# Optimization experiments

Measured on AMD Instinct MI355X. Metric: run time of the kernel, lower is better.

Reference implementation:

```python
import jax, jax.numpy as jnp
import numpy as np
import math

DIM = 1024
N_HEADS = 16
HEAD_DIM = DIM // N_HEADS


def get_sin_cos(seq_len, dim):
    # theta: (dim/2,), freqs: (L, dim/2), emb: (L, dim)
    theta = 10000.0 ** (-jnp.arange(0, dim, 2, dtype=jnp.float32) / dim)
    position = jnp.arange(seq_len, dtype=jnp.float32)
    freqs = position[:, None] * theta[None, :]
    emb = jnp.concatenate([jnp.sin(freqs), jnp.cos(freqs)], axis=-1)
    sin = emb[None, None]  # (1,1,L,dim)
    cos = emb[None, None]
    return sin, cos


def rotate_half(x):
    x1, x2 = x[..., ::2], x[..., 1::2]
    return jnp.concatenate([-x2, x1], axis=-1)


def apply_rope(q, k):
    sin, cos = get_sin_cos(q.shape[2], q.shape[-1])
    q = q * cos + rotate_half(q) * sin
    k = k * cos + rotate_half(k) * sin
    return q, k


def setup_inputs() -> dict:
    key = jax.random.key(0)
    ks = jax.random.split(key, 3)
    B, L, D = 2, 2048, DIM
    x = jax.random.normal(ks[0], (B, L, D), dtype=jnp.float32)
    Wqkv = jax.random.normal(ks[1], (D, 3 * D), dtype=jnp.float32) * (1.0 / math.sqrt(D))
    bqkv = jnp.zeros((3 * D,), dtype=jnp.float32)
    Wout = jax.random.normal(ks[2], (D, D), dtype=jnp.float32) * (1.0 / math.sqrt(D))
    bout = jnp.zeros((D,), dtype=jnp.float32)
    return {"x": x, "Wqkv": Wqkv, "bqkv": bqkv, "Wout": Wout, "bout": bout}


def reference(x, Wqkv, bqkv, Wout, bout):
    B, L, D = x.shape
    H, Hd = N_HEADS, HEAD_DIM
    qkv = (x @ Wqkv + bqkv).reshape(B, L, 3, H, Hd)
    q, k, v = qkv[:, :, 0], qkv[:, :, 1], qkv[:, :, 2]  # (B,L,H,Hd)
    q = q.transpose(0, 2, 1, 3)  # (B,H,L,Hd)
    k = k.transpose(0, 2, 1, 3)
    v = v.transpose(0, 2, 1, 3)
    q, k = apply_rope(q, k)
    scores = jnp.einsum('bhqd,bhkd->bhqk', q, k) / math.sqrt(Hd)
    probs = jax.nn.softmax(scores, axis=-1)
    out = jnp.einsum('bhqk,bhkd->bhqd', probs, v)
    out = out.transpose(0, 2, 1, 3).reshape(B, L, D)
    return out @ Wout + bout
```

## Files before the change

kernel.cpp:

```cpp
#include <hip/hip_runtime.h>
#include <hip/hip_bf16.h>
#include <math.h>

typedef __bf16 bf16;
typedef __bf16 bf16x8 __attribute__((ext_vector_type(8)));
typedef __bf16 bf16x4 __attribute__((ext_vector_type(4)));
typedef float f32x4 __attribute__((ext_vector_type(4)));
typedef float f32x16 __attribute__((ext_vector_type(16)));

#define DEV __device__ __forceinline__
#define AS1(p) ((const __attribute__((address_space(1))) void*)(p))
#define AS3(p) ((__attribute__((address_space(3))) void*)(p))

#define Bsz 2
#define Lseq 2048
#define Dm 1024
#define Hh 16
#define HD 64
#define BL (Bsz * Lseq)
#define TN (3 * Dm)

#define LOG2E 1.44269504088896f

#define OFF_XATT  ((size_t)0)
#define OFF_WQKVT (OFF_XATT  + (size_t)BL * Dm * 2)
#define OFF_WOUTT (OFF_WQKVT + (size_t)TN * Dm * 2)
#define OFF_TAB   (OFF_WOUTT + (size_t)Dm * Dm * 2)
#define OFF_Q     (OFF_TAB   + (size_t)Lseq * 32 * 8)
#define OFF_K     (OFF_Q     + (size_t)BL * Dm * 2)
#define OFF_VT    (OFF_K     + (size_t)BL * Dm * 2)

DEV float exp2_fast(float x) {
    float r;
    asm("v_exp_f32 %0, %1" : "=v"(r) : "v"(x));
    return r;
}

__global__ __launch_bounds__(256) void k_convert(const float* __restrict__ in,
                                                 bf16* __restrict__ out) {
    int i = blockIdx.x * 256 + threadIdx.x;
    const float4* in4 = (const float4*)in;
    float4 a = in4[i * 2];
    float4 b = in4[i * 2 + 1];
    bf16x8 o;
    o[0] = (bf16)a.x; o[1] = (bf16)a.y; o[2] = (bf16)a.z; o[3] = (bf16)a.w;
    o[4] = (bf16)b.x; o[5] = (bf16)b.y; o[6] = (bf16)b.z; o[7] = (bf16)b.w;
    ((bf16x8*)out)[i] = o;
}

__global__ __launch_bounds__(256) void k_transpose(const float* __restrict__ in,
                                                   bf16* __restrict__ out,
                                                   int R, int C) {
    __shared__ float t[32][33];
    int bx = blockIdx.x * 32;
    int by = blockIdx.y * 32;
    int tx = threadIdx.x, ty = threadIdx.y;
#pragma unroll
    for (int i = 0; i < 32; i += 8)
        t[ty + i][tx] = in[(size_t)(by + ty + i) * C + bx + tx];
    __syncthreads();
#pragma unroll
    for (int i = 0; i < 32; i += 8)
        out[(size_t)(bx + ty + i) * R + by + tx] = (bf16)t[tx][ty + i];
}

__global__ __launch_bounds__(256) void k_sincos(float2* __restrict__ tab) {
    int idx = blockIdx.x * 256 + threadIdx.x;
    int pos = idx >> 5, t = idx & 31;
    float theta = powf(10000.0f, -(float)t * (1.0f / 32.0f));
    float f = (float)pos * theta;
    tab[idx] = make_float2(sinf(f), cosf(f));
}

template <int EPI>
DEV void gemm_body(const bf16* __restrict__ A,
                   const bf16* __restrict__ BT,
                   const float* __restrict__ bias,
                   float* __restrict__ C,
                   bf16* __restrict__ qo,
                   bf16* __restrict__ ko,
                   bf16* __restrict__ vt,
                   const float2* __restrict__ tab,
                   int N, int K) {
    __shared__ uint4 smem4[2048];
    char* Al = (char*)smem4;
    char* Bl = (char*)smem4 + 16384;
    const int tid = threadIdx.x;
    const int w = tid >> 6, lane = tid & 63, lg = lane >> 4, lr = lane & 15;
    const int m0 = blockIdx.y * 128, n0 = blockIdx.x * 128;
    const int wm = (w >> 1) * 64, wn = (w & 1) * 64;
    const char* Ab = (const char*)A;
    const char* Bb = (const char*)BT;
    const size_t Kb = (size_t)K * 2;

    f32x4 acc[4][4] = {};

    const int rowL = lane >> 3;
    const int j16 = ((lane & 7) ^ rowL) * 16;

    for (int kt = 0; kt < K; kt += 64) {
#pragma unroll
        for (int c = 0; c < 4; ++c) {
            const int R0 = (w * 4 + c) * 8;
            const int row = R0 + rowL;
            __builtin_amdgcn_global_load_lds(AS1(Ab + (size_t)(m0 + row) * Kb + kt * 2 + j16),
                                             AS3(Al + R0 * 128), 16, 0, 0);
            __builtin_amdgcn_global_load_lds(AS1(Bb + (size_t)(n0 + row) * Kb + kt * 2 + j16),
                                             AS3(Bl + R0 * 128), 16, 0, 0);
        }
        __syncthreads();
#pragma unroll
        for (int kf = 0; kf < 2; ++kf) {
            bf16x8 af[4], bfr[4];
#pragma unroll
            for (int i = 0; i < 4; ++i) {
                int ra = wm + i * 16 + lr;
                af[i] = *(const bf16x8*)(Al + ra * 128 + ((kf * 64 + lg * 16) ^ ((ra & 7) << 4)));
                int rb = wn + i * 16 + lr;
                bfr[i] = *(const bf16x8*)(Bl + rb * 128 + ((kf * 64 + lg * 16) ^ ((rb & 7) << 4)));
            }
#pragma unroll
            for (int i = 0; i < 4; ++i)
#pragma unroll
                for (int j = 0; j < 4; ++j)
                    acc[i][j] = __builtin_amdgcn_mfma_f32_16x16x32_bf16(af[i], bfr[j], acc[i][j], 0, 0, 0);
        }
        __syncthreads();
    }

    if constexpr (EPI == 0) {
#pragma unroll
        for (int i = 0; i < 4; ++i) {
            int row = m0 + wm + i * 16 + lg * 4;
#pragma unroll
            for (int j = 0; j < 4; ++j) {
                int col = n0 + wn + j * 16 + lr;
                float bv = bias[col];
#pragma unroll
                for (int r = 0; r < 4; ++r)
                    C[(size_t)(row + r) * N + col] = acc[i][j][r] + bv;
            }
        }
    } else {
        const int phase = n0 >> 10;
        const int c0 = n0 + wn;
        const int h = (c0 & 1023) >> 6;
        const int b = m0 >> 11;
        const int bh = b * 16 + h;
        const int lbase = (m0 & 2047) + wm;
        float bv[4];
#pragma unroll
        for (int j = 0; j < 4; ++j) bv[j] = bias[c0 + j * 16 + lr];
        float* Lw = (float*)((char*)smem4 + w * 4096);

#pragma unroll
        for (int i = 0; i < 4; ++i) {
#pragma unroll
            for (int j = 0; j < 4; ++j)
#pragma unroll
                for (int r = 0; r < 4; ++r)
                    Lw[(lg * 4 + r) * 64 + j * 16 + lr] = acc[i][j][r] + bv[j];
            __syncthreads();
            if (phase < 2) {
                const float scale = (phase == 0) ? 0.125f * LOG2E : 1.0f;
                bf16* dst = (phase == 0 ? qo : ko) + (size_t)bh * Lseq * 64;
#pragma unroll
                for (int j = 0; j < 4; ++j)
#pragma unroll
                    for (int r = 0; r < 4; ++r) {
                        int rl = lg * 4 + r;
                        int d = j * 16 + lr;
                        int l = lbase + i * 16 + rl;
                        float v = Lw[rl * 64 + d];
                        int dp = (d < 32) ? (2 * d + 1) : (2 * d - 64);
                        float p = Lw[rl * 64 + dp];
                        float2 f = tab[l * 32 + (d & 31)];
                        float val = ((d < 32) ? (v - p) * f.x : (v + p) * f.y) * scale;
                        dst[(size_t)l * 64 + d] = (bf16)val;
                    }
            } else {
                int d = lane;
                int lb = lbase + i * 16;
                bf16x8 o1, o2;
#pragma unroll
                for (int rw = 0; rw < 8; ++rw) {
                    o1[rw] = (bf16)Lw[rw * 64 + d];
                    o2[rw] = (bf16)Lw[(rw + 8) * 64 + d];
                }
                bf16* dst = vt + ((size_t)bh * 64 + d) * Lseq + lb;
                *(bf16x8*)dst = o1;
                *(bf16x8*)(dst + 8) = o2;
            }
            __syncthreads();
        }
    }
}

__global__ __launch_bounds__(256) void k_gemm_qkv(const bf16* __restrict__ A,
                                                  const bf16* __restrict__ BT,
                                                  const float* __restrict__ bias,
                                                  bf16* __restrict__ qo,
                                                  bf16* __restrict__ ko,
                                                  bf16* __restrict__ vt,
                                                  const float2* __restrict__ tab) {
    gemm_body<1>(A, BT, bias, nullptr, qo, ko, vt, tab, TN, Dm);
}
__global__ __launch_bounds__(256) void k_gemm_out(const bf16* __restrict__ A,
                                                  const bf16* __restrict__ BT,
                                                  const float* __restrict__ bias,
                                                  float* __restrict__ C) {
    gemm_body<0>(A, BT, bias, C, nullptr, nullptr, nullptr, nullptr, Dm, Dm);
}

DEV f32x16 mfma32(bf16x8 a, bf16x8 b, f32x16 c) {
    return __builtin_amdgcn_mfma_f32_32x32x16_bf16(a, b, c, 0, 0, 0);
}
DEV unsigned packbf(float lo, float hi) {
    unsigned short a = __builtin_bit_cast(unsigned short, (bf16)lo);
    unsigned short b = __builtin_bit_cast(unsigned short, (bf16)hi);
    return (unsigned)a | ((unsigned)b << 16);
}

DEV void stage_tile(const char* kb, const char* vb, char* Kn, char* Vn,
                    int j0, int qw, int lane) {
#pragma unroll
    for (int c = 0; c < 2; ++c) {
        const int j = qw * 2 + c;
        const int rsw = lane ^ j;
        __builtin_amdgcn_global_load_lds(AS1(kb + (size_t)(j0 + rsw) * 128 + j * 16),
                                         AS3(Kn + j * 1024), 16, 0, 0);
        __builtin_amdgcn_global_load_lds(AS1(vb + (size_t)rsw * 4096 + (size_t)j0 * 2 + j * 16),
                                         AS3(Vn + j * 1024), 16, 0, 0);
    }
}

__global__ __launch_bounds__(512, 4) void k_attn(const bf16* __restrict__ Q,
                                                 const bf16* __restrict__ Kt,
                                                 const bf16* __restrict__ Vt,
                                                 bf16* __restrict__ Op) {
    __shared__ uint4 smem4[4096];
    char* base = (char*)smem4;
    const int tid = threadIdx.x;
    const int w = tid >> 6, lane = tid & 63;
    const int qw = w & 3, s = w >> 2;
    const int hi = lane >> 5, l31 = lane & 31;
    const int bid = blockIdx.x;
    const int bh = bid >> 4, qt = bid & 15;
    const int q0 = qt * 128 + qw * 32;
    const char* qb = (const char*)(Q + (size_t)bh * Lseq * 64);
    const char* kb = (const char*)(Kt + (size_t)bh * Lseq * 64);
    const char* vb = (const char*)(Vt + (size_t)bh * 64 * Lseq);
    char* setb = base + s * 32768;

    bf16x8 qf[4];
#pragma unroll
    for (int kst = 0; kst < 4; ++kst)
        qf[kst] = *(const bf16x8*)(qb + (size_t)(q0 + l31) * 128 + kst * 32 + hi * 16);

    f32x16 o0 = {}, o1 = {};
    float m = -1e30f, lsum = 0.f;

    stage_tile(kb, vb, setb, setb + 8192, s * 16 * 64, qw, lane);
    __syncthreads();

    for (int t = 0; t < 16; ++t) {
        const int cur = t & 1;
        const char* Kl = setb + cur * 16384;
        const char* Vl = Kl + 8192;
        char* Kn = setb + (cur ^ 1) * 16384;
        char* Vn = Kn + 8192;

        if (t < 15) stage_tile(kb, vb, Kn, Vn, (s * 16 + t + 1) * 64, qw, lane);

        f32x16 s0 = {}, s1 = {};
        __builtin_amdgcn_s_setprio(1);
#pragma unroll
        for (int kst = 0; kst < 4; ++kst) {
            const int jK = kst * 2 + hi;
            const int x = l31 ^ jK;
            bf16x8 ka = *(const bf16x8*)(Kl + jK * 1024 + x * 16);
            bf16x8 kc = *(const bf16x8*)(Kl + jK * 1024 + (32 + x) * 16);
            s0 = mfma32(ka, qf[kst], s0);
            s1 = mfma32(kc, qf[kst], s1);
        }
        __builtin_amdgcn_s_setprio(0);

        float pm = fmaxf(s0[0], s0[1]);
#pragma unroll
        for (int r = 2; r < 16; ++r) pm = fmaxf(pm, s0[r]);
#pragma unroll
        for (int r = 0; r < 16; ++r) pm = fmaxf(pm, s1[r]);
        pm = fmaxf(pm, __shfl_xor(pm, 32));
        if (!__all(pm <= m + 8.0f)) {
            float mn = fmaxf(m, pm);
            float sc = exp2_fast(m - mn);
#pragma unroll
            for (int r = 0; r < 16; ++r) { o0[r] *= sc; o1[r] *= sc; }
            lsum *= sc; m = mn;
        }
        float rs = 0.f;
#pragma unroll
        for (int r = 0; r < 16; ++r) { s0[r] = exp2_fast(s0[r] - m); rs += s0[r]; }
#pragma unroll
        for (int r = 0; r < 16; ++r) { s1[r] = exp2_fast(s1[r] - m); rs += s1[r]; }
        rs += __shfl_xor(rs, 32);
        lsum += rs;

        unsigned u[16];
#pragma unroll
        for (int t2 = 0; t2 < 8; ++t2) {
            u[t2]     = packbf(s0[2 * t2], s0[2 * t2 + 1]);
            u[8 + t2] = packbf(s1[2 * t2], s1[2 * t2 + 1]);
        }
        unsigned snd[8], rcv[8];
#pragma unroll
        for (int J = 0; J < 2; ++J)
#pragma unroll
            for (int st = 0; st < 2; ++st) {
                const int t0 = J * 8 + st * 4, q = (J * 2 + st) * 2;
                snd[q + 0] = hi ? u[t0 + 0] : u[t0 + 2];
                snd[q + 1] = hi ? u[t0 + 1] : u[t0 + 3];
            }
#pragma unroll
        for (int t2 = 0; t2 < 8; ++t2) rcv[t2] = __shfl_xor(snd[t2], 32);
        bf16x8 pf[2][2];
#pragma unroll
        for (int J = 0; J < 2; ++J)
#pragma unroll
            for (int st = 0; st < 2; ++st) {
                const int t0 = J * 8 + st * 4, q = (J * 2 + st) * 2;
                union { unsigned wd[4]; bf16x8 v; } f;
                f.wd[0] = hi ? rcv[q + 0] : u[t0 + 0];
                f.wd[1] = hi ? rcv[q + 1] : u[t0 + 1];
                f.wd[2] = hi ? u[t0 + 2] : rcv[q + 0];
                f.wd[3] = hi ? u[t0 + 3] : rcv[q + 1];
                pf[J][st] = f.v;
            }

        __builtin_amdgcn_s_setprio(1);
#pragma unroll
        for (int J = 0; J < 2; ++J)
#pragma unroll
            for (int st = 0; st < 2; ++st) {
                const int jV = J * 4 + st * 2 + hi;
                const int x = l31 ^ jV;
                bf16x8 v0 = *(const bf16x8*)(Vl + jV * 1024 + x * 16);
                bf16x8 v1 = *(const bf16x8*)(Vl + jV * 1024 + (32 + x) * 16);
                o0 = mfma32(v0, pf[J][st], o0);
                o1 = mfma32(v1, pf[J][st], o1);
            }
        __builtin_amdgcn_s_setprio(0);
        __syncthreads();
    }

    float* ex = (float*)base;
    if (s == 1) {
        float* r = ex + qw * 2176;
#pragma unroll
        for (int t = 0; t < 16; ++t) {
            r[t * 64 + lane] = o0[t];
            r[1024 + t * 64 + lane] = o1[t];
        }
        r[2048 + lane] = m;
        r[2112 + lane] = lsum;
    }
    __syncthreads();
    if (s == 0) {
        float* r = ex + qw * 2176;
        const float mb = r[2048 + lane], lb = r[2112 + lane];
        const float M = fmaxf(m, mb);
        const float wa = exp2_fast(m - M), wb = exp2_fast(mb - M);
        const float inv = 1.0f / (wa * lsum + wb * lb);
        const float fa = wa * inv, fb = wb * inv;
        const int b = bh >> 4, h = bh & 15;
        bf16* dst = Op + (size_t)(b * Lseq + q0 + l31) * Dm + h * 64;
#pragma unroll
        for (int t = 0; t < 4; ++t) {
            bf16x4 p0, p1;
#pragma unroll
            for (int i = 0; i < 4; ++i) {
                p0[i] = (bf16)(o0[4 * t + i] * fa + r[(4 * t + i) * 64 + lane] * fb);
                p1[i] = (bf16)(o1[4 * t + i] * fa + r[1024 + (4 * t + i) * 64 + lane] * fb);
            }
            *(bf16x4*)(dst + 8 * t + 4 * hi) = p0;
            *(bf16x4*)(dst + 32 + 8 * t + 4 * hi) = p1;
        }
    }
}

extern "C" void kernel_launch(void* const* d_in, const int* in_sizes, int n_in,
                              void* d_out, int out_size, void* d_ws, size_t ws_size,
                              hipStream_t stream) {
    (void)in_sizes; (void)n_in; (void)out_size; (void)ws_size;
    const float* x    = (const float*)d_in[0];
    const float* Wqkv = (const float*)d_in[1];
    const float* bqkv = (const float*)d_in[2];
    const float* Wout = (const float*)d_in[3];
    const float* bout = (const float*)d_in[4];
    float* out = (float*)d_out;
    char* ws = (char*)d_ws;

    bf16* xbf    = (bf16*)(ws + OFF_XATT);
    bf16* att    = (bf16*)(ws + OFF_XATT);
    bf16* wqkvT  = (bf16*)(ws + OFF_WQKVT);
    bf16* woutT  = (bf16*)(ws + OFF_WOUTT);
    float2* tab  = (float2*)(ws + OFF_TAB);
    bf16* qb     = (bf16*)(ws + OFF_Q);
    bf16* kb     = (bf16*)(ws + OFF_K);
    bf16* vt     = (bf16*)(ws + OFF_VT);

    hipLaunchKernelGGL(k_convert, dim3((BL * Dm) / 8 / 256), dim3(256), 0, stream, x, xbf);
    hipLaunchKernelGGL(k_transpose, dim3(TN / 32, Dm / 32), dim3(32, 8), 0, stream, Wqkv, wqkvT, Dm, TN);
    hipLaunchKernelGGL(k_transpose, dim3(Dm / 32, Dm / 32), dim3(32, 8), 0, stream, Wout, woutT, Dm, Dm);
    hipLaunchKernelGGL(k_sincos, dim3(Lseq * 32 / 256), dim3(256), 0, stream, tab);
    hipLaunchKernelGGL(k_gemm_qkv, dim3(TN / 128, BL / 128), dim3(256), 0, stream,
                       xbf, wqkvT, bqkv, qb, kb, vt, tab);
    hipLaunchKernelGGL(k_attn, dim3(32 * 16), dim3(512), 0, stream, qb, kb, vt, att);
    hipLaunchKernelGGL(k_gemm_out, dim3(Dm / 128, BL / 128), dim3(256), 0, stream,
                       att, woutT, bout, out);
}
```

Baseline: 141.9 us.

## Software-pipeline attention loop: overlap QK of next tile with PV of previous

Restructures the attention inner loop so each iteration issues the QK^T MFMAs for the current key tile alongside the PV MFMAs for the previous tile's probabilities. The softmax of one tile can then overlap with independent matrix work rather than forming a serial dependency chain. This needs a triple-buffered V ring plus a double-buffered K in LDS, so shared memory grows from 64KB to 80KB per block. The max and sum reductions are also rewritten as trees to shorten dependency chains. The cost is more LDS and registers, which may lower occupancy.

```diff
diff --git a/kernel.cpp b/kernel.cpp
--- a/kernel.cpp
+++ b/kernel.cpp
@@ -221,24 +221,126 @@
     return (unsigned)a | ((unsigned)b << 16);
 }
 
-DEV void stage_tile(const char* kb, const char* vb, char* Kn, char* Vn,
-                    int j0, int qw, int lane) {
+DEV void stage_k(const char* kb, char* dst, int j0, int qw, int lane) {
 #pragma unroll
     for (int c = 0; c < 2; ++c) {
         const int j = qw * 2 + c;
         const int rsw = lane ^ j;
         __builtin_amdgcn_global_load_lds(AS1(kb + (size_t)(j0 + rsw) * 128 + j * 16),
-                                         AS3(Kn + j * 1024), 16, 0, 0);
+                                         AS3(dst + j * 1024), 16, 0, 0);
+    }
+}
+DEV void stage_v(const char* vb, char* dst, int j0, int qw, int lane) {
+#pragma unroll
+    for (int c = 0; c < 2; ++c) {
+        const int j = qw * 2 + c;
+        const int rsw = lane ^ j;
         __builtin_amdgcn_global_load_lds(AS1(vb + (size_t)rsw * 4096 + (size_t)j0 * 2 + j * 16),
-                                         AS3(Vn + j * 1024), 16, 0, 0);
-    }
+                                         AS3(dst + j * 1024), 16, 0, 0);
+    }
+}
+
+DEV void qk_cluster(const char* Kl, const bf16x8* qf, int l31, int hi,
+                    f32x16& s0, f32x16& s1) {
+    __builtin_amdgcn_s_setprio(1);
+#pragma unroll
+    for (int kst = 0; kst < 4; ++kst) {
+        const int jK = kst * 2 + hi;
+        const int x = l31 ^ jK;
+        bf16x8 ka = *(const bf16x8*)(Kl + jK * 1024 + x * 16);
+        bf16x8 kc = *(const bf16x8*)(Kl + jK * 1024 + (32 + x) * 16);
+        s0 = mfma32(ka, qf[kst], s0);
+        s1 = mfma32(kc, qf[kst], s1);
+    }
+    __builtin_amdgcn_s_setprio(0);
+}
+
+DEV void pv_cluster(const char* Vl, const bf16x8 pf[2][2], int l31, int hi,
+                    f32x16& o0, f32x16& o1) {
+    __builtin_amdgcn_s_setprio(1);
+#pragma unroll
+    for (int J = 0; J < 2; ++J)
+#pragma unroll
+        for (int st = 0; st < 2; ++st) {
+            const int jV = J * 4 + st * 2 + hi;
+            const int x = l31 ^ jV;
+            bf16x8 v0 = *(const bf16x8*)(Vl + jV * 1024 + x * 16);
+            bf16x8 v1 = *(const bf16x8*)(Vl + jV * 1024 + (32 + x) * 16);
+            o0 = mfma32(v0, pf[J][st], o0);
+            o1 = mfma32(v1, pf[J][st], o1);
+        }
+    __builtin_amdgcn_s_setprio(0);
+}
+
+DEV void softmax_pack(f32x16& s0, f32x16& s1, f32x16& o0, f32x16& o1,
+                      float& m, float& lsum, int hi, bf16x8 pf[2][2]) {
+    float t8[8];
+#pragma unroll
+    for (int i = 0; i < 8; ++i)
+        t8[i] = fmaxf(fmaxf(s0[i], s0[i + 8]), fmaxf(s1[i], s1[i + 8]));
+#pragma unroll
+    for (int i = 0; i < 4; ++i) t8[i] = fmaxf(t8[i], t8[i + 4]);
+    float pm = fmaxf(fmaxf(t8[0], t8[2]), fmaxf(t8[1], t8[3]));
+    pm = fmaxf(pm, __shfl_xor(pm, 32));
+    if (!__all(pm <= m + 8.0f)) {
+        float mn = fmaxf(m, pm);
+        float sc = exp2_fast(m - mn);
+#pragma unroll
+        for (int r = 0; r < 16; ++r) { o0[r] *= sc; o1[r] *= sc; }
+        lsum *= sc; m = mn;
+    }
+#pragma unroll
+    for (int r = 0; r < 16; ++r) s0[r] = exp2_fast(s0[r] - m);
+#pragma unroll
+    for (int r = 0; r < 16; ++r) s1[r] = exp2_fast(s1[r] - m);
+
+    unsigned u[16];
+#pragma unroll
+    for (int t2 = 0; t2 < 8; ++t2) {
+        u[t2]     = packbf(s0[2 * t2], s0[2 * t2 + 1]);
+        u[8 + t2] = packbf(s1[2 * t2], s1[2 * t2 + 1]);
+    }
+    unsigned snd[8], rcv[8];
+#pragma unroll
+    for (int J = 0; J < 2; ++J)
+#pragma unroll
+        for (int st = 0; st < 2; ++st) {
+            const int t0 = J * 8 + st * 4, q = (J * 2 + st) * 2;
+            snd[q + 0] = hi ? u[t0 + 0] : u[t0 + 2];
+            snd[q + 1] = hi ? u[t0 + 1] : u[t0 + 3];
+        }
+#pragma unroll
+    for (int t2 = 0; t2 < 8; ++t2) rcv[t2] = __shfl_xor(snd[t2], 32);
+
+    float r8[8];
+#pragma unroll
+    for (int i = 0; i < 8; ++i)
+        r8[i] = (s0[i] + s0[i + 8]) + (s1[i] + s1[i + 8]);
+#pragma unroll
+    for (int i = 0; i < 4; ++i) r8[i] += r8[i + 4];
+    float rs = (r8[0] + r8[2]) + (r8[1] + r8[3]);
+    rs += __shfl_xor(rs, 32);
+    lsum += rs;
+
+#pragma unroll
+    for (int J = 0; J < 2; ++J)
+#pragma unroll
+        for (int st = 0; st < 2; ++st) {
+            const int t0 = J * 8 + st * 4, q = (J * 2 + st) * 2;
+            union { unsigned wd[4]; bf16x8 v; } f;
+            f.wd[0] = hi ? rcv[q + 0] : u[t0 + 0];
+            f.wd[1] = hi ? rcv[q + 1] : u[t0 + 1];
+            f.wd[2] = hi ? u[t0 + 2] : rcv[q + 0];
+            f.wd[3] = hi ? u[t0 + 3] : rcv[q + 1];
+            pf[J][st] = f.v;
+        }
 }
 
 __global__ __launch_bounds__(512, 4) void k_attn(const bf16* __restrict__ Q,
                                                  const bf16* __restrict__ Kt,
                                                  const bf16* __restrict__ Vt,
                                                  bf16* __restrict__ Op) {
-    __shared__ uint4 smem4[4096];
+    __shared__ uint4 smem4[5120];
     char* base = (char*)smem4;
     const int tid = threadIdx.x;
     const int w = tid >> 6, lane = tid & 63;
@@ -250,7 +352,13 @@
     const char* qb = (const char*)(Q + (size_t)bh * Lseq * 64);
     const char* kb = (const char*)(Kt + (size_t)bh * Lseq * 64);
     const char* vb = (const char*)(Vt + (size_t)bh * 64 * Lseq);
-    char* setb = base + s * 32768;
+    char* setb = base + s * 40960;
+    char* Kb0 = setb;
+    char* Kb1 = setb + 8192;
+    char* VA = setb + 16384;
+    char* VB = setb + 24576;
+    char* VC = setb + 32768;
+    const int jbase = s * 16;
 
     bf16x8 qf[4];
 #pragma unroll
@@ -259,99 +367,39 @@
 
     f32x16 o0 = {}, o1 = {};
     float m = -1e30f, lsum = 0.f;
-
-    stage_tile(kb, vb, setb, setb + 8192, s * 16 * 64, qw, lane);
+    bf16x8 pf[2][2];
+
+    stage_k(kb, Kb0, jbase * 64, qw, lane);
+    stage_v(vb, VA, jbase * 64, qw, lane);
     __syncthreads();
 
-    for (int t = 0; t < 16; ++t) {
-        const int cur = t & 1;
-        const char* Kl = setb + cur * 16384;
-        const char* Vl = Kl + 8192;
-        char* Kn = setb + (cur ^ 1) * 16384;
-        char* Vn = Kn + 8192;
-
-        if (t < 15) stage_tile(kb, vb, Kn, Vn, (s * 16 + t + 1) * 64, qw, lane);
-
-        f32x16 s0 = {}, s1 = {};
-        __builtin_amdgcn_s_setprio(1);
-#pragma unroll
-        for (int kst = 0; kst < 4; ++kst) {
-            const int jK = kst * 2 + hi;
-            const int x = l31 ^ jK;
-            bf16x8 ka = *(const bf16x8*)(Kl + jK * 1024 + x * 16);
-            bf16x8 kc = *(const bf16x8*)(Kl + jK * 1024 + (32 + x) * 16);
-            s0 = mfma32(ka, qf[kst], s0);
-            s1 = mfma32(kc, qf[kst], s1);
-        }
-        __builtin_amdgcn_s_setprio(0);
-
-        float pm = fmaxf(s0[0], s0[1]);
-#pragma unroll
-        for (int r = 2; r < 16; ++r) pm = fmaxf(pm, s0[r]);
-#pragma unroll
-        for (int r = 0; r < 16; ++r) pm = fmaxf(pm, s1[r]);
-        pm = fmaxf(pm, __shfl_xor(pm, 32));
-        if (!__all(pm <= m + 8.0f)) {
-            float mn = fmaxf(m, pm);
-            float sc = exp2_fast(m - mn);
-#pragma unroll
-            for (int r = 0; r < 16; ++r) { o0[r] *= sc; o1[r] *= sc; }
-            lsum *= sc; m = mn;
-        }
-        float rs = 0.f;
-#pragma unroll
-        for (int r = 0; r < 16; ++r) { s0[r] = exp2_fast(s0[r] - m); rs += s0[r]; }
-#pragma unroll
-        for (int r = 0; r < 16; ++r) { s1[r] = exp2_fast(s1[r] - m); rs += s1[r]; }
-        rs += __shfl_xor(rs, 32);
-        lsum += rs;
-
-        unsigned u[16];
-#pragma unroll
-        for (int t2 = 0; t2 < 8; ++t2) {
-            u[t2]     = packbf(s0[2 * t2], s0[2 * t2 + 1]);
-            u[8 + t2] = packbf(s1[2 * t2], s1[2 * t2 + 1]);
-        }
-        unsigned snd[8], rcv[8];
-#pragma unroll
-        for (int J = 0; J < 2; ++J)
-#pragma unroll
-            for (int st = 0; st < 2; ++st) {
-                const int t0 = J * 8 + st * 4, q = (J * 2 + st) * 2;
-                snd[q + 0] = hi ? u[t0 + 0] : u[t0 + 2];
-                snd[q + 1] = hi ? u[t0 + 1] : u[t0 + 3];
-            }
-#pragma unroll
-        for (int t2 = 0; t2 < 8; ++t2) rcv[t2] = __shfl_xor(snd[t2], 32);
-        bf16x8 pf[2][2];
-#pragma unroll
-        for (int J = 0; J < 2; ++J)
-#pragma unroll
-            for (int st = 0; st < 2; ++st) {
-                const int t0 = J * 8 + st * 4, q = (J * 2 + st) * 2;
-                union { unsigned wd[4]; bf16x8 v; } f;
-                f.wd[0] = hi ? rcv[q + 0] : u[t0 + 0];
-                f.wd[1] = hi ? rcv[q + 1] : u[t0 + 1];
-                f.wd[2] = hi ? u[t0 + 2] : rcv[q + 0];
-                f.wd[3] = hi ? u[t0 + 3] : rcv[q + 1];
-                pf[J][st] = f.v;
-            }
-
-        __builtin_amdgcn_s_setprio(1);
-#pragma unroll
-        for (int J = 0; J < 2; ++J)
-#pragma unroll
-            for (int st = 0; st < 2; ++st) {
-                const int jV = J * 4 + st * 2 + hi;
-                const int x = l31 ^ jV;
-                bf16x8 v0 = *(const bf16x8*)(Vl + jV * 1024 + x * 16);
-                bf16x8 v1 = *(const bf16x8*)(Vl + jV * 1024 + (32 + x) * 16);
-                o0 = mfma32(v0, pf[J][st], o0);
-                o1 = mfma32(v1, pf[J][st], o1);
-            }
-        __builtin_amdgcn_s_setprio(0);
+    {
+        stage_k(kb, Kb1, (jbase + 1) * 64, qw, lane);
+        stage_v(vb, VB, (jbase + 1) * 64, qw, lane);
+        f32x16 a0 = {}, a1 = {};
+        qk_cluster(Kb0, qf, l31, hi, a0, a1);
+        softmax_pack(a0, a1, o0, o1, m, lsum, hi, pf);
         __syncthreads();
     }
+
+    char* kcur = Kb1; char* knext = Kb0;
+    char* vprev = VA; char* vcur = VB; char* vnext = VC;
+#pragma unroll 1
+    for (int t = 1; t < 16; ++t) {
+        if (t < 15) {
+            stage_k(kb, knext, (jbase + t + 1) * 64, qw, lane);
+            stage_v(vb, vnext, (jbase + t + 1) * 64, qw, lane);
+        }
+        f32x16 a0 = {}, a1 = {};
+        qk_cluster(kcur, qf, l31, hi, a0, a1);
+        pv_cluster(vprev, pf, l31, hi, o0, o1);
+        softmax_pack(a0, a1, o0, o1, m, lsum, hi, pf);
+        char* tk = kcur; kcur = knext; knext = tk;
+        char* tv = vprev; vprev = vcur; vcur = vnext; vnext = tv;
+        __syncthreads();
+    }
+    pv_cluster(vprev, pf, l31, hi, o0, o1);
+    __syncthreads();
 
     float* ex = (float*)base;
     if (s == 1) {
```

Result: slower. 160.1 us (+12.9%).

## Remap GEMM tiles per XCD and use permlane32 swap in attention

Applied to the files above, without the earlier changes.

Flattens both GEMM grids to 1D and remaps block IDs so that consecutive tiles land on the same XCD, aiming to improve L2 reuse of A/B panels across workgroups. In attention, the cross-half exchange of P values, previously done with __shfl_xor plus selects, now uses v_permlane32_swap, which avoids LDS-based shuffles and the extra select instructions. K and V staging is also split into separate helpers without changing what is loaded. The remapping assumes the grid size is divisible by 8 and that hardware dispatches blocks round-robin across XCDs.

```diff
diff --git a/kernel.cpp b/kernel.cpp
--- a/kernel.cpp
+++ b/kernel.cpp
@@ -34,6 +34,9 @@
     float r;
     asm("v_exp_f32 %0, %1" : "=v"(r) : "v"(x));
     return r;
+}
+DEV void plswap(unsigned& a, unsigned& b) {
+    asm("v_permlane32_swap_b32 %0, %1" : "+v"(a), "+v"(b));
 }
 
 __global__ __launch_bounds__(256) void k_convert(const float* __restrict__ in,
@@ -81,13 +84,12 @@
                    bf16* __restrict__ ko,
                    bf16* __restrict__ vt,
                    const float2* __restrict__ tab,
-                   int N, int K) {
+                   int m0, int n0, int N, int K) {
     __shared__ uint4 smem4[2048];
     char* Al = (char*)smem4;
     char* Bl = (char*)smem4 + 16384;
     const int tid = threadIdx.x;
     const int w = tid >> 6, lane = tid & 63, lg = lane >> 4, lr = lane & 15;
-    const int m0 = blockIdx.y * 128, n0 = blockIdx.x * 128;
     const int wm = (w >> 1) * 64, wn = (w & 1) * 64;
     const char* Ab = (const char*)A;
     const char* Bb = (const char*)BT;
@@ -196,6 +198,13 @@
     }
 }
 
+DEV void xcd_tile(int nx, int nwg, int& m0, int& n0) {
+    int id = blockIdx.x;
+    int id2 = (id & 7) * (nwg >> 3) + (id >> 3);
+    n0 = (id2 % nx) * 128;
+    m0 = (id2 / nx) * 128;
+}
+
 __global__ __launch_bounds__(256) void k_gemm_qkv(const bf16* __restrict__ A,
                                                   const bf16* __restrict__ BT,
                                                   const float* __restrict__ bias,
@@ -203,13 +212,17 @@
                                                   bf16* __restrict__ ko,
                                                   bf16* __restrict__ vt,
                                                   const float2* __restrict__ tab) {
-    gemm_body<1>(A, BT, bias, nullptr, qo, ko, vt, tab, TN, Dm);
+    int m0, n0;
+    xcd_tile(TN / 128, (TN / 128) * (BL / 128), m0, n0);
+    gemm_body<1>(A, BT, bias, nullptr, qo, ko, vt, tab, m0, n0, TN, Dm);
 }
 __global__ __launch_bounds__(256) void k_gemm_out(const bf16* __restrict__ A,
                                                   const bf16* __restrict__ BT,
                                                   const float* __restrict__ bias,
                                                   float* __restrict__ C) {
-    gemm_body<0>(A, BT, bias, C, nullptr, nullptr, nullptr, nullptr, Dm, Dm);
+    int m0, n0;
+    xcd_tile(Dm / 128, (Dm / 128) * (BL / 128), m0, n0);
+    gemm_body<0>(A, BT, bias, C, nullptr, nullptr, nullptr, nullptr, m0, n0, Dm, Dm);
 }
 
 DEV f32x16 mfma32(bf16x8 a, bf16x8 b, f32x16 c) {
@@ -221,16 +234,22 @@
     return (unsigned)a | ((unsigned)b << 16);
 }
 
-DEV void stage_tile(const char* kb, const char* vb, char* Kn, char* Vn,
-                    int j0, int qw, int lane) {
+DEV void stage_k(const char* kb, char* dst, int j0, int qw, int lane) {
 #pragma unroll
     for (int c = 0; c < 2; ++c) {
         const int j = qw * 2 + c;
         const int rsw = lane ^ j;
         __builtin_amdgcn_global_load_lds(AS1(kb + (size_t)(j0 + rsw) * 128 + j * 16),
-                                         AS3(Kn + j * 1024), 16, 0, 0);
+                                         AS3(dst + j * 1024), 16, 0, 0);
+    }
+}
+DEV void stage_v(const char* vb, char* dst, int j0, int qw, int lane) {
+#pragma unroll
+    for (int c = 0; c < 2; ++c) {
+        const int j = qw * 2 + c;
+        const int rsw = lane ^ j;
         __builtin_amdgcn_global_load_lds(AS1(vb + (size_t)rsw * 4096 + (size_t)j0 * 2 + j * 16),
-                                         AS3(Vn + j * 1024), 16, 0, 0);
+                                         AS3(dst + j * 1024), 16, 0, 0);
     }
 }
 
@@ -251,6 +270,7 @@
     const char* kb = (const char*)(Kt + (size_t)bh * Lseq * 64);
     const char* vb = (const char*)(Vt + (size_t)bh * 64 * Lseq);
     char* setb = base + s * 32768;
+    const int jbase = s * 16;
 
     bf16x8 qf[4];
 #pragma unroll
@@ -260,7 +280,8 @@
     f32x16 o0 = {}, o1 = {};
     float m = -1e30f, lsum = 0.f;
 
-    stage_tile(kb, vb, setb, setb + 8192, s * 16 * 64, qw, lane);
+    stage_k(kb, setb, jbase * 64, qw, lane);
+    stage_v(vb, setb + 8192, jbase * 64, qw, lane);
     __syncthreads();
 
     for (int t = 0; t < 16; ++t) {
@@ -270,7 +291,10 @@
         char* Kn = setb + (cur ^ 1) * 16384;
         char* Vn = Kn + 8192;
 
-        if (t < 15) stage_tile(kb, vb, Kn, Vn, (s * 16 + t + 1) * 64, qw, lane);
+        if (t < 15) {
+            stage_k(kb, Kn, (jbase + t + 1) * 64, qw, lane);
+            stage_v(vb, Vn, (jbase + t + 1) * 64, qw, lane);
+        }
 
         f32x16 s0 = {}, s1 = {};
         __builtin_amdgcn_s_setprio(1);
@@ -312,28 +336,19 @@
             u[t2]     = packbf(s0[2 * t2], s0[2 * t2 + 1]);
             u[8 + t2] = packbf(s1[2 * t2], s1[2 * t2 + 1]);
         }
-        unsigned snd[8], rcv[8];
+        bf16x8 pf[2][2];
 #pragma unroll
         for (int J = 0; J < 2; ++J)
 #pragma unroll
             for (int st = 0; st < 2; ++st) {
-                const int t0 = J * 8 + st * 4, q = (J * 2 + st) * 2;
-                snd[q + 0] = hi ? u[t0 + 0] : u[t0 + 2];
-                snd[q + 1] = hi ? u[t0 + 1] : u[t0 + 3];
-            }
-#pragma unroll
-        for (int t2 = 0; t2 < 8; ++t2) rcv[t2] = __shfl_xor(snd[t2], 32);
-        bf16x8 pf[2][2];
-#pragma unroll
-        for (int J = 0; J < 2; ++J)
-#pragma unroll
-            for (int st = 0; st < 2; ++st) {
-                const int t0 = J * 8 + st * 4, q = (J * 2 + st) * 2;
+                const int t0 = J * 8 + st * 4;
+                plswap(u[t0 + 0], u[t0 + 2]);
+                plswap(u[t0 + 1], u[t0 + 3]);
                 union { unsigned wd[4]; bf16x8 v; } f;
-                f.wd[0] = hi ? rcv[q + 0] : u[t0 + 0];
-                f.wd[1] = hi ? rcv[q + 1] : u[t0 + 1];
-                f.wd[2] = hi ? u[t0 + 2] : rcv[q + 0];
-                f.wd[3] = hi ? u[t0 + 3] : rcv[q + 1];
+                f.wd[0] = u[t0 + 0];
+                f.wd[1] = u[t0 + 1];
+                f.wd[2] = u[t0 + 2];
+                f.wd[3] = u[t0 + 3];
                 pf[J][st] = f.v;
             }
 
@@ -413,9 +428,9 @@
     hipLaunchKernelGGL(k_transpose, dim3(TN / 32, Dm / 32), dim3(32, 8), 0, stream, Wqkv, wqkvT, Dm, TN);
     hipLaunchKernelGGL(k_transpose, dim3(Dm / 32, Dm / 32), dim3(32, 8), 0, stream, Wout, woutT, Dm, Dm);
     hipLaunchKernelGGL(k_sincos, dim3(Lseq * 32 / 256), dim3(256), 0, stream, tab);
-    hipLaunchKernelGGL(k_gemm_qkv, dim3(TN / 128, BL / 128), dim3(256), 0, stream,
+    hipLaunchKernelGGL(k_gemm_qkv, dim3((TN / 128) * (BL / 128)), dim3(256), 0, stream,
                        xbf, wqkvT, bqkv, qb, kb, vt, tab);
     hipLaunchKernelGGL(k_attn, dim3(32 * 16), dim3(512), 0, stream, qb, kb, vt, att);
-    hipLaunchKernelGGL(k_gemm_out, dim3(Dm / 128, BL / 128), dim3(256), 0, stream,
+    hipLaunchKernelGGL(k_gemm_out, dim3((Dm / 128) * (BL / 128)), dim3(256), 0, stream,
                        att, woutT, bout, out);
 }
```

Measured after the change: 137.5 us. -3.1%, faster.
